# Kernel tuning notes

Measured on AMD Instinct MI355X. Metric: run time of the kernel, lower is better.

The kernel has to match this reference:

```python
import jax, jax.numpy as jnp
import numpy as np

HEAD_DIM = 64
N_KV_HEADS = 4


def _rope(t, cos, sin):
    # t: (B, S, H, HD); cos/sin: (S, HD//2); interleaved (real, imag) pairs
    tr = t.astype(jnp.float32).reshape(*t.shape[:-1], -1, 2)
    xr, xi = tr[..., 0], tr[..., 1]
    c = cos[None, :, None, :]
    s = sin[None, :, None, :]
    out_r = xr * c - xi * s
    out_i = xr * s + xi * c
    return jnp.stack([out_r, out_i], axis=-1).reshape(t.shape).astype(t.dtype)


def setup_inputs() -> dict:
    key = jax.random.key(0)
    ks = jax.random.split(key, 5)
    B, S, D = 2, 2048, 1024
    kv_dim = N_KV_HEADS * HEAD_DIM  # 256
    x = jax.random.normal(ks[0], (B, S, D), jnp.float32)
    wq = jax.random.normal(ks[1], (D, D), jnp.float32) * 0.02
    wk = jax.random.normal(ks[2], (kv_dim, D), jnp.float32) * 0.02
    wv = jax.random.normal(ks[3], (kv_dim, D), jnp.float32) * 0.02
    wo = jax.random.normal(ks[4], (D, D), jnp.float32) * 0.02
    # precompute_freqs_cis (LLaMA): theta = 10000
    half = HEAD_DIM // 2
    inv_freq = 1.0 / (10000.0 ** (np.arange(0, HEAD_DIM, 2).astype(np.float32) / HEAD_DIM))
    ang = np.outer(np.arange(S, dtype=np.float32), inv_freq)  # (S, half)
    freqs_cos = jnp.asarray(np.cos(ang), jnp.float32)
    freqs_sin = jnp.asarray(np.sin(ang), jnp.float32)
    return {"x": x, "wq": wq, "wk": wk, "wv": wv, "wo": wo,
            "freqs_cos": freqs_cos, "freqs_sin": freqs_sin}


def reference(x, wq, wk, wv, wo, freqs_cos, freqs_sin):
    B, S, D = x.shape
    HD = HEAD_DIM
    HKV = N_KV_HEADS
    H = D // HD
    NREP = H // HKV
    # QKV projections (torch Linear: y = x @ W.T)
    xq = jnp.einsum('bsd,od->bso', x, wq).reshape(B, S, H, HD)
    xk = jnp.einsum('bsd,od->bso', x, wk).reshape(B, S, HKV, HD)
    xv = jnp.einsum('bsd,od->bso', x, wv).reshape(B, S, HKV, HD)
    # RoPE (complex multiply on interleaved pairs)
    xq = _rope(xq, freqs_cos, freqs_sin)
    xk = _rope(xk, freqs_cos, freqs_sin)
    # GQA: group query heads by kv head instead of materializing repeated KV
    xq = xq.reshape(B, S, HKV, NREP, HD)
    scale = 1.0 / jnp.sqrt(jnp.asarray(HD, jnp.float32))
    scores = jnp.einsum('bqkrh,bskh->bkrqs', xq, xk) * scale  # (B,HKV,NREP,S,S)
    causal = jnp.tril(jnp.ones((S, S), bool))
    scores = jnp.where(causal, scores, jnp.finfo(scores.dtype).min)
    probs = jax.nn.softmax(scores, axis=-1)
    out = jnp.einsum('bkrqs,bskh->bqkrh', probs, xv).reshape(B, S, H * HD)
    return jnp.einsum('bso,do->bsd', out, wo)
```

## Files before the change

### kernel.cpp

```cpp
#include <hip/hip_runtime.h>
#include <hip/hip_bf16.h>

typedef __attribute__((ext_vector_type(8))) short short8;
typedef __attribute__((ext_vector_type(4))) float floatx4;
typedef __attribute__((ext_vector_type(4))) float float4v;
typedef __attribute__((ext_vector_type(4))) unsigned short ushort4v;

#define S_LEN 2048
#define D_MODEL 1024
#define HD 64
#define HQ 16
#define HKV 4

__device__ __forceinline__ unsigned short f2bf(float f) {
    unsigned int u = __builtin_bit_cast(unsigned int, f);
    u += 0x7fffu + ((u >> 16) & 1u);
    return (unsigned short)(u >> 16);
}

__device__ __forceinline__ unsigned int cvt_pk_bf16(float lo, float hi) {
    unsigned int r;
    asm volatile("v_cvt_pk_bf16_f32 %0, %1, %2" : "=v"(r) : "v"(lo), "v"(hi));
    return r;
}

__device__ __forceinline__ void gload16(const unsigned short* g, unsigned short* l) {
    __builtin_amdgcn_global_load_lds(
        (const __attribute__((address_space(1))) void*)g,
        (__attribute__((address_space(3))) void*)l, 16, 0, 0);
}

__global__ void cvt_f32_bf16(const float* __restrict__ in, unsigned short* __restrict__ out, int n) {
    int i = (blockIdx.x * blockDim.x + threadIdx.x) * 4;
    int stride = gridDim.x * blockDim.x * 4;
    for (; i < n; i += stride) {
        float4v v = *(const float4v*)(in + i);
        ushort4v o;
        o.x = f2bf(v.x); o.y = f2bf(v.y); o.z = f2bf(v.z); o.w = f2bf(v.w);
        *(ushort4v*)(out + i) = o;
    }
}

template<int EPI>
__global__ __launch_bounds__(256) void gemm128(
    const unsigned short* __restrict__ A, const unsigned short* __restrict__ W,
    float* __restrict__ C,
    unsigned short* __restrict__ Qb, unsigned short* __restrict__ Kb, unsigned short* __restrict__ Vtb,
    const float* __restrict__ fcos, const float* __restrict__ fsin,
    int K, int N)
{
    __shared__ __align__(16) unsigned short Asm[128 * 64];
    __shared__ __align__(16) unsigned short Bsm[128 * 64];

    const int tid  = threadIdx.x;
    const int lane = tid & 63;
    const int w    = tid >> 6;
    const int wr   = w >> 1, wc = w & 1;
    const int l15  = lane & 15, lhi = lane >> 4;
    const int row0 = blockIdx.x * 128;
    const int col0 = blockIdx.y * 128;

    const int r_in = tid >> 3;
    const int sp   = tid & 7;
    const int sl   = sp ^ (r_in & 7);

    floatx4 acc[4][4] = {};

    for (int k0 = 0; k0 < K; k0 += 64) {
        #pragma unroll
        for (int i = 0; i < 4; i++) {
            const int r = i * 32 + r_in;
            gload16(A + (size_t)(row0 + r) * K + k0 + sl * 8, Asm + i * 2048 + w * 512);
            gload16(W + (size_t)(col0 + r) * K + k0 + sl * 8, Bsm + i * 2048 + w * 512);
        }
        __syncthreads();

        short8 af[4][2], bfr[4][2];
        const int rx = l15 & 7;
        #pragma unroll
        for (int mi = 0; mi < 4; mi++) {
            const int rowa = wr * 64 + mi * 16 + l15;
            const int rowb = wc * 64 + mi * 16 + l15;
            #pragma unroll
            for (int ks = 0; ks < 2; ks++) {
                const int slot = (ks * 4 + lhi) ^ rx;
                af[mi][ks]  = *(const short8*)&Asm[rowa * 64 + slot * 8];
                bfr[mi][ks] = *(const short8*)&Bsm[rowb * 64 + slot * 8];
            }
        }

        __builtin_amdgcn_s_setprio(1);
        #pragma unroll
        for (int mi = 0; mi < 4; mi++)
        #pragma unroll
        for (int ni = 0; ni < 4; ni++) {
            acc[mi][ni] = __builtin_amdgcn_mfma_f32_16x16x32_bf16(af[mi][0], bfr[ni][0], acc[mi][ni], 0, 0, 0);
            acc[mi][ni] = __builtin_amdgcn_mfma_f32_16x16x32_bf16(af[mi][1], bfr[ni][1], acc[mi][ni], 0, 0, 0);
        }
        __builtin_amdgcn_s_setprio(0);
        __syncthreads();
    }

    #pragma unroll
    for (int mi = 0; mi < 4; mi++)
    #pragma unroll
    for (int ni = 0; ni < 4; ni++)
    #pragma unroll
    for (int j = 0; j < 4; j++) {
        const int row = row0 + wr * 64 + mi * 16 + lhi * 4 + j;
        const int col = col0 + wc * 64 + ni * 16 + l15;
        float v = acc[mi][ni][j];
        if (EPI == 0) {
            C[(size_t)row * D_MODEL + col] = v;
        } else {
            if (col0 < D_MODEL) {
                float pv = __shfl_xor(v, 1);
                int s  = row & (S_LEN - 1);
                int fi = (col & (HD - 1)) >> 1;
                float c  = fcos[s * (HD / 2) + fi];
                float sn = fsin[s * (HD / 2) + fi];
                float o = (col & 1) ? (pv * sn + v * c) : (v * c - pv * sn);
                Qb[(size_t)row * D_MODEL + col] = f2bf(o);
            } else if (col0 < D_MODEL + 256) {
                int ck = col - D_MODEL;
                float pv = __shfl_xor(v, 1);
                int s  = row & (S_LEN - 1);
                int fi = (ck & (HD - 1)) >> 1;
                float c  = fcos[s * (HD / 2) + fi];
                float sn = fsin[s * (HD / 2) + fi];
                float o = (ck & 1) ? (pv * sn + v * c) : (v * c - pv * sn);
                Kb[(size_t)row * 256 + ck] = f2bf(o);
            } else {
                int cv = col - (D_MODEL + 256);
                int b = row >> 11, s = row & (S_LEN - 1);
                int kvh = cv >> 6, d = cv & (HD - 1);
                Vtb[((size_t)(b * HKV + kvh) * HD + d) * S_LEN + s] = f2bf(v);
            }
        }
    }
}

__global__ __launch_bounds__(64) void flash_attn(
    const unsigned short* __restrict__ Q, const unsigned short* __restrict__ Kk,
    const unsigned short* __restrict__ Vt, unsigned short* __restrict__ O)
{
    const int lane = threadIdx.x;
    const int l15 = lane & 15, lhi = lane >> 4;
    const int bid = blockIdx.x;
    const int h  = bid & 15;
    const int b  = (bid >> 4) & 1;
    const int qc = 63 - (bid >> 5);
    const int kvh = h >> 2;
    const int qbase = qc * 32;

    __shared__ __align__(16) unsigned short plds[2][16][72];

    short8 qf[2][2];
    #pragma unroll
    for (int qi = 0; qi < 2; qi++) {
        const unsigned short* qp =
            Q + ((size_t)(b * S_LEN + qbase + qi * 16 + l15) * HQ + h) * HD + lhi * 8;
        qf[qi][0] = *(const short8*)qp;
        qf[qi][1] = *(const short8*)(qp + 32);
    }

    floatx4 oacc[2][4] = {};
    float m_run[2] = {-1e30f, -1e30f};
    float l_run[2] = {0.f, 0.f};

    const unsigned short* kbase = Kk + ((size_t)(b * S_LEN) * HKV + kvh) * HD + lhi * 8;
    const unsigned short* vbase = Vt + (size_t)((b * HKV + kvh) * HD + l15) * S_LEN + lhi * 8;

    for (int s0 = 0; s0 <= qbase + 31; s0 += 64) {
        short8 kf[4][2];
        #pragma unroll
        for (int st = 0; st < 4; st++) {
            const unsigned short* kp = kbase + (size_t)(s0 + st * 16 + l15) * (HKV * HD);
            kf[st][0] = *(const short8*)kp;
            kf[st][1] = *(const short8*)(kp + 32);
        }
        short8 vf[4][2];
        #pragma unroll
        for (int dct = 0; dct < 4; dct++) {
            const unsigned short* vp = vbase + (size_t)(dct * 16) * S_LEN + s0;
            vf[dct][0] = *(const short8*)vp;
            vf[dct][1] = *(const short8*)(vp + 32);
        }

        #pragma unroll
        for (int qi = 0; qi < 2; qi++) {
            const int qb = qbase + qi * 16;
            if (s0 > qb) continue;

            floatx4 sacc[4] = {};
            __builtin_amdgcn_s_setprio(1);
            #pragma unroll
            for (int st = 0; st < 4; st++) {
                sacc[st] = __builtin_amdgcn_mfma_f32_16x16x32_bf16(kf[st][0], qf[qi][0], sacc[st], 0, 0, 0);
                sacc[st] = __builtin_amdgcn_mfma_f32_16x16x32_bf16(kf[st][1], qf[qi][1], sacc[st], 0, 0, 0);
            }
            __builtin_amdgcn_s_setprio(0);

            const int q = qb + l15;
            if (s0 + 63 > qb) {
                #pragma unroll
                for (int st = 0; st < 4; st++)
                #pragma unroll
                for (int j = 0; j < 4; j++) {
                    int s = s0 + st * 16 + lhi * 4 + j;
                    if (s > q) sacc[st][j] = -1e30f;
                }
            }

            float rmax = sacc[0][0];
            #pragma unroll
            for (int st = 0; st < 4; st++)
            #pragma unroll
            for (int j = 0; j < 4; j++) rmax = fmaxf(rmax, sacc[st][j]);
            rmax = fmaxf(rmax, __shfl_xor(rmax, 16));
            rmax = fmaxf(rmax, __shfl_xor(rmax, 32));
            float rscale = rmax * 0.125f;

            if (!__all(rscale <= m_run[qi] + 8.0f)) {
                float mnew = fmaxf(m_run[qi], rscale);
                float rr = __expf(m_run[qi] - mnew);
                m_run[qi] = mnew;
                l_run[qi] *= rr;
                #pragma unroll
                for (int dct = 0; dct < 4; dct++)
                #pragma unroll
                for (int j = 0; j < 4; j++) oacc[qi][dct][j] *= rr;
            }
            const float mcur = m_run[qi];

            float psum = 0.f;
            unsigned int pk[4][2];
            #pragma unroll
            for (int st = 0; st < 4; st++) {
                float p0 = __expf(fmaf(sacc[st][0], 0.125f, -mcur));
                float p1 = __expf(fmaf(sacc[st][1], 0.125f, -mcur));
                float p2 = __expf(fmaf(sacc[st][2], 0.125f, -mcur));
                float p3 = __expf(fmaf(sacc[st][3], 0.125f, -mcur));
                psum += (p0 + p1) + (p2 + p3);
                pk[st][0] = cvt_pk_bf16(p0, p1);
                pk[st][1] = cvt_pk_bf16(p2, p3);
            }
            psum += __shfl_xor(psum, 16);
            psum += __shfl_xor(psum, 32);
            l_run[qi] += psum;

            #pragma unroll
            for (int st = 0; st < 4; st++) {
                *(unsigned int*)&plds[qi][l15][st * 16 + lhi * 4 + 0] = pk[st][0];
                *(unsigned int*)&plds[qi][l15][st * 16 + lhi * 4 + 2] = pk[st][1];
            }
            short8 pf0 = *(const short8*)&plds[qi][l15][lhi * 8];
            short8 pf1 = *(const short8*)&plds[qi][l15][32 + lhi * 8];

            __builtin_amdgcn_s_setprio(1);
            #pragma unroll
            for (int dct = 0; dct < 4; dct++) {
                oacc[qi][dct] = __builtin_amdgcn_mfma_f32_16x16x32_bf16(vf[dct][0], pf0, oacc[qi][dct], 0, 0, 0);
                oacc[qi][dct] = __builtin_amdgcn_mfma_f32_16x16x32_bf16(vf[dct][1], pf1, oacc[qi][dct], 0, 0, 0);
            }
            __builtin_amdgcn_s_setprio(0);
        }
    }

    #pragma unroll
    for (int qi = 0; qi < 2; qi++) {
        float rl = 1.0f / l_run[qi];
        const int q = qbase + qi * 16 + l15;
        unsigned short* op = O + ((size_t)(b * S_LEN + q) * HQ + h) * HD + lhi * 4;
        #pragma unroll
        for (int dct = 0; dct < 4; dct++) {
            unsigned int w0 = cvt_pk_bf16(oacc[qi][dct][0] * rl, oacc[qi][dct][1] * rl);
            unsigned int w1 = cvt_pk_bf16(oacc[qi][dct][2] * rl, oacc[qi][dct][3] * rl);
            *(unsigned int*)(op + dct * 16)     = w0;
            *(unsigned int*)(op + dct * 16 + 2) = w1;
        }
    }
}

extern "C" void kernel_launch(void* const* d_in, const int* in_sizes, int n_in,
                              void* d_out, int out_size, void* d_ws, size_t ws_size,
                              hipStream_t stream) {
    const float* x    = (const float*)d_in[0];
    const float* wq   = (const float*)d_in[1];
    const float* wk   = (const float*)d_in[2];
    const float* wv   = (const float*)d_in[3];
    const float* wo   = (const float*)d_in[4];
    const float* fcos = (const float*)d_in[5];
    const float* fsin = (const float*)d_in[6];
    float* out = (float*)d_out;

    char* ws = (char*)d_ws;
    unsigned short* xb    = (unsigned short*)(ws);
    unsigned short* wqkvb = (unsigned short*)(ws + 8388608);
    unsigned short* wob   = (unsigned short*)(ws + 11534336);
    unsigned short* Qb    = (unsigned short*)(ws + 13631488);
    unsigned short* Kb    = (unsigned short*)(ws + 22020096);
    unsigned short* Vtb   = (unsigned short*)(ws + 24117248);
    unsigned short* Ab    = (unsigned short*)(ws + 26214400);

    cvt_f32_bf16<<<1024, 256, 0, stream>>>(x,  xb, 4096 * 1024);
    cvt_f32_bf16<<<256,  256, 0, stream>>>(wq, wqkvb,              1024 * 1024);
    cvt_f32_bf16<<<64,   256, 0, stream>>>(wk, wqkvb + 1024 * 1024, 256 * 1024);
    cvt_f32_bf16<<<64,   256, 0, stream>>>(wv, wqkvb + 1280 * 1024, 256 * 1024);
    cvt_f32_bf16<<<256,  256, 0, stream>>>(wo, wob,                1024 * 1024);

    gemm128<1><<<dim3(32, 12), 256, 0, stream>>>(xb, wqkvb, nullptr, Qb, Kb, Vtb,
                                                 fcos, fsin, 1024, 1536);

    flash_attn<<<64 * 32, 64, 0, stream>>>(Qb, Kb, Vtb, Ab);

    gemm128<0><<<dim3(32, 8), 256, 0, stream>>>(Ab, wob, out, nullptr, nullptr, nullptr,
                                                nullptr, nullptr, 1024, 1024);
}
```

Measured before the change: 150.4 us.

## Split attention KV loop across two waves, prescale Q for exp2, merge weight casts

Each attention block now has two waves that take alternating 64-key tiles and combine their partial softmax states through LDS at the end. This halves the serial KV loop per block. The softmax scale and log2(e) are folded into Q in the projection epilogue so the inner loop can call the hardware exp2 directly without an fma. The four weight-conversion launches are merged into one kernel. The cost is more LDS, a block barrier, and a final merge step, and Q is rounded to bf16 after scaling.

```diff
diff --git a/kernel.cpp b/kernel.cpp
--- a/kernel.cpp
+++ b/kernel.cpp
@@ -11,6 +11,7 @@
 #define HD 64
 #define HQ 16
 #define HKV 4
+#define QK_PRESCALE 0.18033688011112042f
 
 __device__ __forceinline__ unsigned short f2bf(float f) {
     unsigned int u = __builtin_bit_cast(unsigned int, f);
@@ -21,6 +22,12 @@
 __device__ __forceinline__ unsigned int cvt_pk_bf16(float lo, float hi) {
     unsigned int r;
     asm volatile("v_cvt_pk_bf16_f32 %0, %1, %2" : "=v"(r) : "v"(lo), "v"(hi));
+    return r;
+}
+
+__device__ __forceinline__ float exp2_hw(float x) {
+    float r;
+    asm("v_exp_f32 %0, %1" : "=v"(r) : "v"(x));
     return r;
 }
 
@@ -39,6 +46,21 @@
         o.x = f2bf(v.x); o.y = f2bf(v.y); o.z = f2bf(v.z); o.w = f2bf(v.w);
         *(ushort4v*)(out + i) = o;
     }
+}
+
+__global__ void cvt_weights(const float* __restrict__ wq, const float* __restrict__ wk,
+                            const float* __restrict__ wv, const float* __restrict__ wo,
+                            unsigned short* __restrict__ dst) {
+    int i = (blockIdx.x * blockDim.x + threadIdx.x) * 4;
+    const float* src; int off;
+    if (i < 1048576)      { src = wq; off = i; }
+    else if (i < 1310720) { src = wk; off = i - 1048576; }
+    else if (i < 1572864) { src = wv; off = i - 1310720; }
+    else                  { src = wo; off = i - 1572864; }
+    float4v v = *(const float4v*)(src + off);
+    ushort4v o;
+    o.x = f2bf(v.x); o.y = f2bf(v.y); o.z = f2bf(v.z); o.w = f2bf(v.w);
+    *(ushort4v*)(dst + i) = o;
 }
 
 template<int EPI>
@@ -120,7 +142,7 @@
                 float c  = fcos[s * (HD / 2) + fi];
                 float sn = fsin[s * (HD / 2) + fi];
                 float o = (col & 1) ? (pv * sn + v * c) : (v * c - pv * sn);
-                Qb[(size_t)row * D_MODEL + col] = f2bf(o);
+                Qb[(size_t)row * D_MODEL + col] = f2bf(o * QK_PRESCALE);
             } else if (col0 < D_MODEL + 256) {
                 int ck = col - D_MODEL;
                 float pv = __shfl_xor(v, 1);
@@ -140,11 +162,13 @@
     }
 }
 
-__global__ __launch_bounds__(64) void flash_attn(
+__global__ __launch_bounds__(128, 4) void flash_attn(
     const unsigned short* __restrict__ Q, const unsigned short* __restrict__ Kk,
     const unsigned short* __restrict__ Vt, unsigned short* __restrict__ O)
 {
-    const int lane = threadIdx.x;
+    const int tid  = threadIdx.x;
+    const int lane = tid & 63;
+    const int wid  = tid >> 6;
     const int l15 = lane & 15, lhi = lane >> 4;
     const int bid = blockIdx.x;
     const int h  = bid & 15;
@@ -154,6 +178,8 @@
     const int qbase = qc * 32;
 
     __shared__ __align__(16) unsigned short plds[2][16][72];
+    __shared__ __align__(16) float Olds[32][64];
+    __shared__ float mlds[2][16], llds[2][16];
 
     short8 qf[2][2];
     #pragma unroll
@@ -171,7 +197,10 @@
     const unsigned short* kbase = Kk + ((size_t)(b * S_LEN) * HKV + kvh) * HD + lhi * 8;
     const unsigned short* vbase = Vt + (size_t)((b * HKV + kvh) * HD + l15) * S_LEN + lhi * 8;
 
-    for (int s0 = 0; s0 <= qbase + 31; s0 += 64) {
+    const int nt = (qbase + 31) / 64 + 1;
+
+    for (int t = wid; t < nt; t += 2) {
+        const int s0 = t * 64;
         short8 kf[4][2];
         #pragma unroll
         for (int st = 0; st < 4; st++) {
@@ -219,11 +248,10 @@
             for (int j = 0; j < 4; j++) rmax = fmaxf(rmax, sacc[st][j]);
             rmax = fmaxf(rmax, __shfl_xor(rmax, 16));
             rmax = fmaxf(rmax, __shfl_xor(rmax, 32));
-            float rscale = rmax * 0.125f;
-
-            if (!__all(rscale <= m_run[qi] + 8.0f)) {
-                float mnew = fmaxf(m_run[qi], rscale);
-                float rr = __expf(m_run[qi] - mnew);
+
+            if (!__all(rmax <= m_run[qi] + 8.0f)) {
+                float mnew = fmaxf(m_run[qi], rmax);
+                float rr = exp2_hw(m_run[qi] - mnew);
                 m_run[qi] = mnew;
                 l_run[qi] *= rr;
                 #pragma unroll
@@ -237,10 +265,10 @@
             unsigned int pk[4][2];
             #pragma unroll
             for (int st = 0; st < 4; st++) {
-                float p0 = __expf(fmaf(sacc[st][0], 0.125f, -mcur));
-                float p1 = __expf(fmaf(sacc[st][1], 0.125f, -mcur));
-                float p2 = __expf(fmaf(sacc[st][2], 0.125f, -mcur));
-                float p3 = __expf(fmaf(sacc[st][3], 0.125f, -mcur));
+                float p0 = exp2_hw(sacc[st][0] - mcur);
+                float p1 = exp2_hw(sacc[st][1] - mcur);
+                float p2 = exp2_hw(sacc[st][2] - mcur);
+                float p3 = exp2_hw(sacc[st][3] - mcur);
                 psum += (p0 + p1) + (p2 + p3);
                 pk[st][0] = cvt_pk_bf16(p0, p1);
                 pk[st][1] = cvt_pk_bf16(p2, p3);
@@ -251,11 +279,11 @@
 
             #pragma unroll
             for (int st = 0; st < 4; st++) {
-                *(unsigned int*)&plds[qi][l15][st * 16 + lhi * 4 + 0] = pk[st][0];
-                *(unsigned int*)&plds[qi][l15][st * 16 + lhi * 4 + 2] = pk[st][1];
-            }
-            short8 pf0 = *(const short8*)&plds[qi][l15][lhi * 8];
-            short8 pf1 = *(const short8*)&plds[qi][l15][32 + lhi * 8];
+                *(unsigned int*)&plds[wid][l15][st * 16 + lhi * 4 + 0] = pk[st][0];
+                *(unsigned int*)&plds[wid][l15][st * 16 + lhi * 4 + 2] = pk[st][1];
+            }
+            short8 pf0 = *(const short8*)&plds[wid][l15][lhi * 8];
+            short8 pf1 = *(const short8*)&plds[wid][l15][32 + lhi * 8];
 
             __builtin_amdgcn_s_setprio(1);
             #pragma unroll
@@ -267,17 +295,38 @@
         }
     }
 
-    #pragma unroll
-    for (int qi = 0; qi < 2; qi++) {
-        float rl = 1.0f / l_run[qi];
-        const int q = qbase + qi * 16 + l15;
-        unsigned short* op = O + ((size_t)(b * S_LEN + q) * HQ + h) * HD + lhi * 4;
-        #pragma unroll
-        for (int dct = 0; dct < 4; dct++) {
-            unsigned int w0 = cvt_pk_bf16(oacc[qi][dct][0] * rl, oacc[qi][dct][1] * rl);
-            unsigned int w1 = cvt_pk_bf16(oacc[qi][dct][2] * rl, oacc[qi][dct][3] * rl);
-            *(unsigned int*)(op + dct * 16)     = w0;
-            *(unsigned int*)(op + dct * 16 + 2) = w1;
+    if (wid == 1) {
+        #pragma unroll
+        for (int qi = 0; qi < 2; qi++) {
+            if (lhi == 0) { mlds[qi][l15] = m_run[qi]; llds[qi][l15] = l_run[qi]; }
+            #pragma unroll
+            for (int dct = 0; dct < 4; dct++)
+            #pragma unroll
+            for (int j = 0; j < 4; j++)
+                Olds[qi * 16 + dct * 4 + j][lane] = oacc[qi][dct][j];
+        }
+    }
+    __syncthreads();
+    if (wid == 0) {
+        #pragma unroll
+        for (int qi = 0; qi < 2; qi++) {
+            float m1 = mlds[qi][l15], l1 = llds[qi][l15];
+            float m  = fmaxf(m_run[qi], m1);
+            float f0 = exp2_hw(m_run[qi] - m);
+            float f1 = exp2_hw(m1 - m);
+            float rl = 1.0f / (l_run[qi] * f0 + l1 * f1);
+            float s0f = f0 * rl, s1f = f1 * rl;
+            const int q = qbase + qi * 16 + l15;
+            unsigned short* op = O + ((size_t)(b * S_LEN + q) * HQ + h) * HD + lhi * 4;
+            #pragma unroll
+            for (int dct = 0; dct < 4; dct++) {
+                float o0 = oacc[qi][dct][0] * s0f + Olds[qi * 16 + dct * 4 + 0][lane] * s1f;
+                float o1 = oacc[qi][dct][1] * s0f + Olds[qi * 16 + dct * 4 + 1][lane] * s1f;
+                float o2 = oacc[qi][dct][2] * s0f + Olds[qi * 16 + dct * 4 + 2][lane] * s1f;
+                float o3 = oacc[qi][dct][3] * s0f + Olds[qi * 16 + dct * 4 + 3][lane] * s1f;
+                *(unsigned int*)(op + dct * 16)     = cvt_pk_bf16(o0, o1);
+                *(unsigned int*)(op + dct * 16 + 2) = cvt_pk_bf16(o2, o3);
+            }
         }
     }
 }
@@ -303,16 +352,13 @@
     unsigned short* Vtb   = (unsigned short*)(ws + 24117248);
     unsigned short* Ab    = (unsigned short*)(ws + 26214400);
 
-    cvt_f32_bf16<<<1024, 256, 0, stream>>>(x,  xb, 4096 * 1024);
-    cvt_f32_bf16<<<256,  256, 0, stream>>>(wq, wqkvb,              1024 * 1024);
-    cvt_f32_bf16<<<64,   256, 0, stream>>>(wk, wqkvb + 1024 * 1024, 256 * 1024);
-    cvt_f32_bf16<<<64,   256, 0, stream>>>(wv, wqkvb + 1280 * 1024, 256 * 1024);
-    cvt_f32_bf16<<<256,  256, 0, stream>>>(wo, wob,                1024 * 1024);
+    cvt_f32_bf16<<<1024, 256, 0, stream>>>(x, xb, 4096 * 1024);
+    cvt_weights<<<2560, 256, 0, stream>>>(wq, wk, wv, wo, wqkvb);
 
     gemm128<1><<<dim3(32, 12), 256, 0, stream>>>(xb, wqkvb, nullptr, Qb, Kb, Vtb,
                                                  fcos, fsin, 1024, 1536);
 
-    flash_attn<<<64 * 32, 64, 0, stream>>>(Qb, Kb, Vtb, Ab);
+    flash_attn<<<64 * 32, 128, 0, stream>>>(Qb, Kb, Vtb, Ab);
 
     gemm128<0><<<dim3(32, 8), 256, 0, stream>>>(Ab, wob, out, nullptr, nullptr, nullptr,
                                                 nullptr, nullptr, 1024, 1024);
```

New measurement: 220.0 us. +46.3%, slower.
